# Kernel optimization log

Measured on AMD Instinct MI355X. Metric: run time of the kernel, lower is better.

## Reference

```python
import jax, jax.numpy as jnp
import numpy as np
import math

T, B, D, H, FF = 2048, 2, 1024, 16, 4096
HD = D // H
STD = 0.02


def _gelu(x):
    # SongNet gelu: tanh approximation
    return 0.5 * x * (1.0 + jnp.tanh(math.sqrt(2.0 / math.pi) * (x + 0.044715 * x ** 3)))


def _layer_norm(x, g, b, eps=1e-5):
    mu = jnp.mean(x, axis=-1, keepdims=True)
    var = jnp.mean((x - mu) ** 2, axis=-1, keepdims=True)
    return (x - mu) * jax.lax.rsqrt(var + eps) * g + b


def setup_inputs() -> dict:
    key = jax.random.key(0)
    ks = jax.random.split(key, 6)
    return {
        "x": jax.random.normal(ks[0], (T, B, D), jnp.float32),
        "attn_mask": jnp.triu(jnp.ones((T, T), bool), k=1),  # True = masked (causal)
        "in_proj_w": jax.random.normal(ks[1], (3 * D, D), jnp.float32) * STD,
        "in_proj_b": jnp.zeros((3 * D,), jnp.float32),
        "out_w": jax.random.normal(ks[2], (D, D), jnp.float32) * STD,
        "out_b": jnp.zeros((D,), jnp.float32),
        "fc1_w": jax.random.normal(ks[3], (FF, D), jnp.float32) * STD,
        "fc1_b": jnp.zeros((FF,), jnp.float32),
        "fc2_w": jax.random.normal(ks[4], (D, FF), jnp.float32) * STD,
        "fc2_b": jnp.zeros((D,), jnp.float32),
        "ln1_g": jnp.ones((D,), jnp.float32),
        "ln1_b": jnp.zeros((D,), jnp.float32),
        "ln2_g": jnp.ones((D,), jnp.float32),
        "ln2_b": jnp.zeros((D,), jnp.float32),
    }


def reference(x, attn_mask, in_proj_w, in_proj_b, out_w, out_b,
              fc1_w, fc1_b, fc2_w, fc2_b, ln1_g, ln1_b, ln2_g, ln2_b):
    t, b, d = x.shape
    scaling = HD ** -0.5
    # fused in-proj (qkv_same path): [T,B,3D]
    qkv = x @ in_proj_w.T + in_proj_b
    q, k, v = jnp.split(qkv, 3, axis=-1)
    q = q * scaling

    def to_heads(z):  # [T,B,D] -> [B*H, T, HD]
        return z.reshape(t, b * H, HD).transpose(1, 0, 2)

    q, k, v = to_heads(q), to_heads(k), to_heads(v)
    # [B*H, T, T] attention scores (full matrix, as in original bmm)
    scores = jnp.einsum('nth,nsh->nts', q, k)
    scores = jnp.where(attn_mask[None, :, :], -jnp.inf, scores)
    w = jax.nn.softmax(scores, axis=-1)
    attn = jnp.einsum('nts,nsh->nth', w, v)          # [B*H, T, HD]
    attn = attn.transpose(1, 0, 2).reshape(t, b, d)  # [T,B,D]
    attn = attn @ out_w.T + out_b

    h = _layer_norm(x + attn, ln1_g, ln1_b)
    ff = _gelu(h @ fc1_w.T + fc1_b) @ fc2_w.T + fc2_b
    out = _layer_norm(h + ff, ln2_g, ln2_b)
    return out
```

## Files before the change

### kernel.cpp

```cpp
#include <hip/hip_runtime.h>
#include <hip/hip_bf16.h>
#include <math.h>


typedef __bf16 bf16x8_t __attribute__((ext_vector_type(8)));
typedef __bf16 bf16x4_t __attribute__((ext_vector_type(4)));
typedef __bf16 bf16x2_t __attribute__((ext_vector_type(2)));
typedef float  f32x4_t  __attribute__((ext_vector_type(4)));

#define T_  2048
#define B_  2
#define D_  1024
#define H_  16
#define HD_ 64
#define FF_ 4096
#define M_  (T_ * B_)

#define LOG2E 1.4426950408889634f
#define SCL   (0.125f * LOG2E)

__device__ __forceinline__ float gelu_f(float v) {
    const float y = 0.79788456080286535588f * (v + 0.044715f * v * v * v);
    const float t = __builtin_amdgcn_exp2f(-2.8853900817779268f * y);
    return v * __builtin_amdgcn_rcpf(1.0f + t);
}

__device__ __forceinline__ void gld_lds16(const void* g, void* l) {
    __builtin_amdgcn_global_load_lds((const __attribute__((address_space(1))) void*)g,
                                     (__attribute__((address_space(3))) void*)l, 16, 0, 0);
}

template<int MODE, int OWNM, int VT>
__global__ __launch_bounds__(256, 4)
void gemm_bt(const __bf16* __restrict__ A, const __bf16* __restrict__ W,
             const float* __restrict__ bias, float* __restrict__ Cf0,
             float* __restrict__ Cf1, __bf16* __restrict__ Cb,
             __bf16* __restrict__ vt, int M, int N, int K)
{
    __shared__ __align__(16) __bf16 As[128 * 64];
    __shared__ __align__(16) __bf16 Bs[128 * 64];
    const int tid  = threadIdx.x;
    const int lane = tid & 63;
    const int wave = tid >> 6;
    const int quad = lane >> 4;
    const int l15  = lane & 15;

    const int gx = gridDim.x, gy = gridDim.y;
    int flat = ((int)blockIdx.z * gy + (int)blockIdx.y) * gx + (int)blockIdx.x;
    int bx, by, z;
    if (OWNM) {
        const int P = gy >> 3;
        const int x = flat & 7; int s = flat >> 3;
        by = x * P + (s % P); s /= P;
        bx = s % gx; z = s / gx;
    } else {
        const int P = gx >> 3;
        const int x = flat & 7; int s = flat >> 3;
        bx = x * P + (s % P); s /= P;
        by = s % gy; z = s / gy;
    }
    const int m0 = by * 128;
    const int n0 = bx * 128;
    const int wm = (wave >> 1) * 64;
    const int wn = (wave & 1) * 64;
    const int Kloc = K / (int)gridDim.z;
    const int kbeg = z * Kloc;

    const int srow8 = lane >> 3;
    const int scol  = ((lane & 7) ^ srow8) * 8;
    const __bf16* gA = A + (size_t)(m0 + wave * 32 + srow8) * K + scol;
    const __bf16* gB = W + (size_t)(n0 + wave * 32 + srow8) * K + scol;
    const size_t row8K = (size_t)8 * K;
    __bf16* ldsA = As + wave * 2048;
    __bf16* ldsB = Bs + wave * 2048;

    const int fsw = l15 & 7;

    f32x4_t acc[4][4] = {};

    for (int kb = kbeg; kb < kbeg + Kloc; kb += 64) {
        #pragma unroll
        for (int j = 0; j < 4; ++j) {
            gld_lds16(gA + kb + j * row8K, ldsA + j * 512);
            gld_lds16(gB + kb + j * row8K, ldsB + j * 512);
        }
        __syncthreads();
        #pragma unroll
        for (int half = 0; half < 2; ++half) {
            const int co = ((quad + half * 4) ^ fsw) * 8;
            bf16x8_t af[4], bfr[4];
            #pragma unroll
            for (int i = 0; i < 4; ++i) af[i]  = *(const bf16x8_t*)&As[(wm + i * 16 + l15) * 64 + co];
            #pragma unroll
            for (int i = 0; i < 4; ++i) bfr[i] = *(const bf16x8_t*)&Bs[(wn + i * 16 + l15) * 64 + co];
            #pragma unroll
            for (int mi = 0; mi < 4; ++mi)
                #pragma unroll
                for (int ni = 0; ni < 4; ++ni)
                    acc[mi][ni] = __builtin_amdgcn_mfma_f32_16x16x32_bf16(af[mi], bfr[ni], acc[mi][ni], 0, 0, 0);
        }
        __syncthreads();
    }

    float* __restrict__ Cf = (z == 0) ? Cf0 : Cf1;
    #pragma unroll
    for (int mi = 0; mi < 4; ++mi) {
        const int row = m0 + wm + mi * 16 + quad * 4;
        #pragma unroll
        for (int ni = 0; ni < 4; ++ni) {
            const int col = n0 + wn + ni * 16 + l15;
            const float bv = (z == 0) ? bias[col] : 0.f;
            float v[4];
            #pragma unroll
            for (int r = 0; r < 4; ++r) {
                v[r] = acc[mi][ni][r] + bv;
                if (MODE == 2) v[r] = gelu_f(v[r]);
            }
            if (MODE == 0) {
                #pragma unroll
                for (int r = 0; r < 4; ++r) Cf[(size_t)(row + r) * N + col] = v[r];
            } else {
                #pragma unroll
                for (int r = 0; r < 4; ++r) Cb[(size_t)(row + r) * N + col] = (__bf16)v[r];
            }
            if (VT && n0 >= 2 * D_) {
                const int colv = col - 2 * D_;
                const int h2 = colv >> 6, hd = colv & 63;
                const int t0 = row >> 1;
                bf16x2_t p0 = {(__bf16)v[0], (__bf16)v[2]};
                bf16x2_t p1 = {(__bf16)v[1], (__bf16)v[3]};
                *(bf16x2_t*)(vt + ((size_t)(h2 * 64 + hd)) * T_ + t0) = p0;
                *(bf16x2_t*)(vt + ((size_t)((H_ + h2) * 64 + hd)) * T_ + t0) = p1;
            }
        }
    }
}

struct QState {
    bf16x8_t aq0, aq1;
    f32x4_t  o[4];
    float    lsum;
};

__device__ __forceinline__ void attn_tile_step(
    QState& st, const __bf16* __restrict__ Ks, const __bf16* __restrict__ Vs,
    __bf16* __restrict__ Psw, bool diag, int wave, int quad, int l15, int ksw)
{
    f32x4_t scT[4] = {};
    #pragma unroll
    for (int ni = 0; ni < 4; ++ni) {
        const int rb = (ni * 16 + l15) * 64;
        bf16x8_t kf0 = *(const bf16x8_t*)&Ks[rb + ((quad ^ ksw) & 7) * 8];
        bf16x8_t kf1 = *(const bf16x8_t*)&Ks[rb + (((quad + 4) ^ ksw) & 7) * 8];
        scT[ni] = __builtin_amdgcn_mfma_f32_16x16x32_bf16(kf0, st.aq0, scT[ni], 0, 0, 0);
        scT[ni] = __builtin_amdgcn_mfma_f32_16x16x32_bf16(kf1, st.aq1, scT[ni], 0, 0, 0);
    }
    float rsum = 0.f;
    #pragma unroll
    for (int ni = 0; ni < 4; ++ni) {
        bf16x4_t pk;
        #pragma unroll
        for (int r = 0; r < 4; ++r) {
            float pv = __builtin_amdgcn_exp2f(scT[ni][r] * SCL);
            if (diag) {
                const int sl = ni * 16 + quad * 4 + r;
                pv = (sl <= wave * 16 + l15) ? pv : 0.f;
            }
            rsum += pv;
            pk[r] = (__bf16)pv;
        }
        *(bf16x4_t*)&Psw[l15 * 64 + ((ni * 4 + quad + l15) & 15) * 4] = pk;
    }
    rsum += __shfl_xor(rsum, 16, 64);
    rsum += __shfl_xor(rsum, 32, 64);
    st.lsum += rsum;

    const int rowb = l15 * 64;
    bf16x4_t a0 = *(const bf16x4_t*)&Psw[rowb + ((quad * 2     + l15) & 15) * 4];
    bf16x4_t a1 = *(const bf16x4_t*)&Psw[rowb + ((quad * 2 + 1 + l15) & 15) * 4];
    bf16x4_t a2 = *(const bf16x4_t*)&Psw[rowb + ((quad * 2 + 8 + l15) & 15) * 4];
    bf16x4_t a3 = *(const bf16x4_t*)&Psw[rowb + ((quad * 2 + 9 + l15) & 15) * 4];
    bf16x8_t ap0 = __builtin_shufflevector(a0, a1, 0, 1, 2, 3, 4, 5, 6, 7);
    bf16x8_t ap1 = __builtin_shufflevector(a2, a3, 0, 1, 2, 3, 4, 5, 6, 7);

    #pragma unroll
    for (int ni = 0; ni < 4; ++ni) {
        const int rbv = (ni * 16 + l15) * 64;
        bf16x8_t bv0 = *(const bf16x8_t*)&Vs[rbv + ((quad ^ ksw) & 7) * 8];
        bf16x8_t bv1 = *(const bf16x8_t*)&Vs[rbv + (((quad + 4) ^ ksw) & 7) * 8];
        st.o[ni] = __builtin_amdgcn_mfma_f32_16x16x32_bf16(ap0, bv0, st.o[ni], 0, 0, 0);
        st.o[ni] = __builtin_amdgcn_mfma_f32_16x16x32_bf16(ap1, bv1, st.o[ni], 0, 0, 0);
    }
}

__global__ __launch_bounds__(256)
void attn_kernel(const __bf16* __restrict__ qkv, const __bf16* __restrict__ vt,
                 __bf16* __restrict__ attnout)
{
    const int bh = blockIdx.y;
    const int b  = bh >> 4;
    const int h  = bh & 15;
    const int tid  = threadIdx.x;
    const int lane = tid & 63;
    const int wave = tid >> 6;
    const int quad = lane >> 4;
    const int l15  = lane & 15;

    __shared__ __align__(16) __bf16 Ks[64 * 64];
    __shared__ __align__(16) __bf16 Vs[64 * 64];
    __shared__ __align__(16) __bf16 Ps[4][16 * 64];

    const int kr = lane >> 3;
    const int kc = (lane & 7) ^ kr;
    const size_t krow = (size_t)B_ * 3 * D_;
    const __bf16* gK0 = qkv + ((size_t)(wave * 16 + kr) * B_ + b) * (3 * D_) + D_ + h * HD_ + kc * 8;
    const __bf16* gV0 = vt + ((size_t)bh * 64 + wave * 16 + kr) * T_ + kc * 8;
    __bf16* ldsK0 = &Ks[wave * 16 * 64];
    __bf16* ldsK1 = &Ks[wave * 16 * 64 + 8 * 64];
    __bf16* ldsV0 = &Vs[wave * 16 * 64];
    __bf16* ldsV1 = &Vs[wave * 16 * 64 + 8 * 64];
    const int ksw = l15 & 7;
    __bf16* Psw = &Ps[wave][0];

    const int qtA = 31 - (int)blockIdx.x;
    const int qtB = (int)blockIdx.x;

    QState stA = {}, stB = {};
    {
        const int tqA = qtA * 64 + wave * 16 + l15;
        const __bf16* qbA = qkv + ((size_t)tqA * B_ + b) * (3 * D_) + h * HD_;
        stA.aq0 = *(const bf16x8_t*)(qbA + quad * 8);
        stA.aq1 = *(const bf16x8_t*)(qbA + 32 + quad * 8);
        const int tqB = qtB * 64 + wave * 16 + l15;
        const __bf16* qbB = qkv + ((size_t)tqB * B_ + b) * (3 * D_) + h * HD_;
        stB.aq0 = *(const bf16x8_t*)(qbB + quad * 8);
        stB.aq1 = *(const bf16x8_t*)(qbB + 32 + quad * 8);
    }

    for (int kt = 0; kt <= qtA; ++kt) {
        const int s0 = kt * 64;
        __syncthreads();
        gld_lds16(gK0 + (size_t)s0 * krow,       ldsK0);
        gld_lds16(gK0 + (size_t)(s0 + 8) * krow, ldsK1);
        gld_lds16(gV0 + s0,                      ldsV0);
        gld_lds16(gV0 + (size_t)8 * T_ + s0,     ldsV1);
        __syncthreads();

        attn_tile_step(stA, Ks, Vs, Psw, kt == qtA, wave, quad, l15, ksw);
        if (kt <= qtB)
            attn_tile_step(stB, Ks, Vs, Psw, kt == qtB, wave, quad, l15, ksw);
    }

    #pragma unroll
    for (int t = 0; t < 2; ++t) {
        const QState& st = t ? stB : stA;
        const int q0 = (t ? qtB : qtA) * 64;
        float linv[4];
        #pragma unroll
        for (int r = 0; r < 4; ++r)
            linv[r] = __builtin_amdgcn_rcpf(__shfl(st.lsum, quad * 4 + r, 64));
        #pragma unroll
        for (int ni = 0; ni < 4; ++ni) {
            #pragma unroll
            for (int r = 0; r < 4; ++r) {
                const int tr = q0 + wave * 16 + quad * 4 + r;
                attnout[((size_t)tr * B_ + b) * D_ + h * HD_ + ni * 16 + l15] =
                    (__bf16)(st.o[ni][r] * linv[r]);
            }
        }
    }
}

template<int AF32, int WF, int WB>
__global__ __launch_bounds__(256)
void ln3_kernel(const void* __restrict__ Ap, const float* __restrict__ R0,
                const float* __restrict__ R1,
                const float* __restrict__ g, const float* __restrict__ bb,
                float* __restrict__ outf, __bf16* __restrict__ outb)
{
    const int row = blockIdx.x;
    const int tid = threadIdx.x;
    float a0, a1, a2, a3;
    if (AF32) {
        const float4 va = ((const float4*)((const float*)Ap + (size_t)row * D_))[tid];
        a0 = va.x; a1 = va.y; a2 = va.z; a3 = va.w;
    } else {
        const bf16x4_t va = ((const bf16x4_t*)((const __bf16*)Ap + (size_t)row * D_))[tid];
        a0 = (float)va[0]; a1 = (float)va[1]; a2 = (float)va[2]; a3 = (float)va[3];
    }
    const float4 v0 = ((const float4*)(R0 + (size_t)row * D_))[tid];
    const float4 v1 = ((const float4*)(R1 + (size_t)row * D_))[tid];
    const float z0 = a0 + v0.x + v1.x, z1 = a1 + v0.y + v1.y;
    const float z2 = a2 + v0.z + v1.z, z3 = a3 + v0.w + v1.w;
    float s  = z0 + z1 + z2 + z3;
    float ss = z0 * z0 + z1 * z1 + z2 * z2 + z3 * z3;
    #pragma unroll
    for (int off = 1; off < 64; off <<= 1) {
        s  += __shfl_xor(s, off, 64);
        ss += __shfl_xor(ss, off, 64);
    }
    __shared__ float rs[4], rss[4];
    const int wv = tid >> 6, lane = tid & 63;
    if (lane == 0) { rs[wv] = s; rss[wv] = ss; }
    __syncthreads();
    s  = rs[0] + rs[1] + rs[2] + rs[3];
    ss = rss[0] + rss[1] + rss[2] + rss[3];
    const float mu   = s * (1.f / D_);
    const float var  = ss * (1.f / D_) - mu * mu;
    const float rstd = rsqrtf(var + 1e-5f);
    const float4 vg = ((const float4*)g)[tid];
    const float4 vb = ((const float4*)bb)[tid];
    const float o0 = (z0 - mu) * rstd * vg.x + vb.x;
    const float o1 = (z1 - mu) * rstd * vg.y + vb.y;
    const float o2 = (z2 - mu) * rstd * vg.z + vb.z;
    const float o3 = (z3 - mu) * rstd * vg.w + vb.w;
    if (WF) ((float4*)(outf + (size_t)row * D_))[tid] = make_float4(o0, o1, o2, o3);
    if (WB) {
        bf16x4_t ob;
        ob[0] = (__bf16)o0; ob[1] = (__bf16)o1; ob[2] = (__bf16)o2; ob[3] = (__bf16)o3;
        ((bf16x4_t*)(outb + (size_t)row * D_))[tid] = ob;
    }
}

__global__ __launch_bounds__(256)
void cvt3_kernel(const float* __restrict__ s0, __bf16* __restrict__ d0, int n0,
                 const float* __restrict__ s1, __bf16* __restrict__ d1, int n1,
                 const float* __restrict__ s2, __bf16* __restrict__ d2, int n2)
{
    int i = blockIdx.x * 256 + threadIdx.x;
    const float* s; __bf16* d;
    if (i < n0) { s = s0; d = d0; }
    else if ((i -= n0) < n1) { s = s1; d = d1; }
    else if ((i -= n1) < n2) { s = s2; d = d2; }
    else return;
    const float4 v = ((const float4*)s)[i];
    bf16x4_t ob;
    ob[0] = (__bf16)v.x; ob[1] = (__bf16)v.y; ob[2] = (__bf16)v.z; ob[3] = (__bf16)v.w;
    ((bf16x4_t*)d)[i] = ob;
}

extern "C" void kernel_launch(void* const* d_in, const int* in_sizes, int n_in,
                              void* d_out, int out_size, void* d_ws, size_t ws_size,
                              hipStream_t stream)
{
    (void)in_sizes; (void)n_in; (void)out_size; (void)ws_size;
    const float* x         = (const float*)d_in[0];
    const float* in_proj_w = (const float*)d_in[2];
    const float* in_proj_b = (const float*)d_in[3];
    const float* out_w     = (const float*)d_in[4];
    const float* out_b     = (const float*)d_in[5];
    const float* fc1_w     = (const float*)d_in[6];
    const float* fc1_b     = (const float*)d_in[7];
    const float* fc2_w     = (const float*)d_in[8];
    const float* fc2_b     = (const float*)d_in[9];
    const float* ln1_g     = (const float*)d_in[10];
    const float* ln1_b     = (const float*)d_in[11];
    const float* ln2_g     = (const float*)d_in[12];
    const float* ln2_b     = (const float*)d_in[13];

    char* p = (char*)d_ws;
    __bf16* regA = (__bf16*)p; p += (size_t)M_ * D_ * 2;
    __bf16* hb   = (__bf16*)p; p += (size_t)M_ * D_ * 2;
    __bf16* wreg = (__bf16*)p; p += (size_t)FF_ * D_ * 2;
    __bf16* qkvb = (__bf16*)p;
    __bf16* g1b  = qkvb;       p += (size_t)M_ * FF_ * 2;
    float*  yf   = (float*)p;  p += (size_t)M_ * D_ * 4;
    float*  hf   = (float*)p;  p += (size_t)M_ * D_ * 4;
    __bf16* vt    = (__bf16*)yf;
    __bf16* outwb = wreg + (size_t)3 * D_ * D_;
    __bf16* fc2wb = (__bf16*)hf;
    float*  ff1   = (float*)d_out;

    const dim3 blk(256);

    {
        const int nx = M_ * D_ / 4, ni = 3 * D_ * D_ / 4, no = D_ * D_ / 4;
        cvt3_kernel<<<dim3((nx + ni + no) / 256), blk, 0, stream>>>(
            x, regA, nx, in_proj_w, wreg, ni, out_w, outwb, no);
    }

    gemm_bt<1, 1, 1><<<dim3(3 * D_ / 128, M_ / 128, 1), blk, 0, stream>>>(
        regA, wreg, in_proj_b, nullptr, nullptr, qkvb, vt, M_, 3 * D_, D_);

    attn_kernel<<<dim3(T_ / 128, B_ * H_), blk, 0, stream>>>(qkvb, vt, regA);

    gemm_bt<0, 1, 0><<<dim3(D_ / 128, M_ / 128, 2), blk, 0, stream>>>(
        regA, outwb, out_b, yf, hf, nullptr, nullptr, M_, D_, D_);

    ln3_kernel<1, 0, 1><<<dim3(M_), blk, 0, stream>>>(x, yf, hf, ln1_g, ln1_b, nullptr, hb);

    cvt3_kernel<<<dim3((2 * FF_ * D_ / 4) / 256), blk, 0, stream>>>(
        fc1_w, wreg, FF_ * D_ / 4, fc2_w, fc2wb, D_ * FF_ / 4, nullptr, nullptr, 0);

    gemm_bt<2, 0, 0><<<dim3(FF_ / 128, M_ / 128, 1), blk, 0, stream>>>(
        hb, wreg, fc1_b, nullptr, nullptr, g1b, nullptr, M_, FF_, D_);

    gemm_bt<0, 1, 0><<<dim3(D_ / 128, M_ / 128, 2), blk, 0, stream>>>(
        g1b, fc2wb, fc2_b, yf, ff1, nullptr, nullptr, M_, D_, FF_);

    ln3_kernel<0, 1, 0><<<dim3(M_), blk, 0, stream>>>(hb, yf, ff1, ln2_g, ln2_b, (float*)d_out, nullptr);
}
```

Baseline: 329.1 us.

## Double-buffer K/V tiles and interleave both query tiles per attention step

The attention kernel now keeps two LDS buffers for K and V. While the current tile is being computed, it prefetches the next tile, which removes the second barrier and the exposed global-to-LDS load latency in each iteration. The two per-block query tiles (A and B) are also processed together in one fused step with separate P scratch buffers. Their independent MFMA and exp chains can then interleave for more instruction-level parallelism. The cost is twice the LDS for K, V and P and more live registers, which may reduce occupancy.

After: 335.6 us. About the same (+2.0%).

```diff
diff --git a/kernel.cpp b/kernel.cpp
--- a/kernel.cpp
+++ b/kernel.cpp
@@ -142,54 +142,97 @@
     float    lsum;
 };
 
-__device__ __forceinline__ void attn_tile_step(
-    QState& st, const __bf16* __restrict__ Ks, const __bf16* __restrict__ Vs,
-    __bf16* __restrict__ Psw, bool diag, int wave, int quad, int l15, int ksw)
-{
-    f32x4_t scT[4] = {};
+__device__ __forceinline__ void attn_dual_step(
+    QState& stA, QState& stB, bool doB, bool diagA, bool diagB,
+    const __bf16* __restrict__ Ks, const __bf16* __restrict__ Vs,
+    __bf16* __restrict__ PsA, __bf16* __restrict__ PsB,
+    int wave, int quad, int l15, int ksw)
+{
+    f32x4_t scA[4] = {}, scB[4] = {};
     #pragma unroll
     for (int ni = 0; ni < 4; ++ni) {
         const int rb = (ni * 16 + l15) * 64;
         bf16x8_t kf0 = *(const bf16x8_t*)&Ks[rb + ((quad ^ ksw) & 7) * 8];
         bf16x8_t kf1 = *(const bf16x8_t*)&Ks[rb + (((quad + 4) ^ ksw) & 7) * 8];
-        scT[ni] = __builtin_amdgcn_mfma_f32_16x16x32_bf16(kf0, st.aq0, scT[ni], 0, 0, 0);
-        scT[ni] = __builtin_amdgcn_mfma_f32_16x16x32_bf16(kf1, st.aq1, scT[ni], 0, 0, 0);
-    }
-    float rsum = 0.f;
+        scA[ni] = __builtin_amdgcn_mfma_f32_16x16x32_bf16(kf0, stA.aq0, scA[ni], 0, 0, 0);
+        scA[ni] = __builtin_amdgcn_mfma_f32_16x16x32_bf16(kf1, stA.aq1, scA[ni], 0, 0, 0);
+        if (doB) {
+            scB[ni] = __builtin_amdgcn_mfma_f32_16x16x32_bf16(kf0, stB.aq0, scB[ni], 0, 0, 0);
+            scB[ni] = __builtin_amdgcn_mfma_f32_16x16x32_bf16(kf1, stB.aq1, scB[ni], 0, 0, 0);
+        }
+    }
+    float rsumA = 0.f, rsumB = 0.f;
     #pragma unroll
     for (int ni = 0; ni < 4; ++ni) {
-        bf16x4_t pk;
+        const int slot = ((ni * 4 + quad + l15) & 15) * 4;
+        bf16x4_t pkA;
         #pragma unroll
         for (int r = 0; r < 4; ++r) {
-            float pv = __builtin_amdgcn_exp2f(scT[ni][r] * SCL);
-            if (diag) {
+            float pv = __builtin_amdgcn_exp2f(scA[ni][r] * SCL);
+            if (diagA) {
                 const int sl = ni * 16 + quad * 4 + r;
                 pv = (sl <= wave * 16 + l15) ? pv : 0.f;
             }
-            rsum += pv;
-            pk[r] = (__bf16)pv;
-        }
-        *(bf16x4_t*)&Psw[l15 * 64 + ((ni * 4 + quad + l15) & 15) * 4] = pk;
-    }
-    rsum += __shfl_xor(rsum, 16, 64);
-    rsum += __shfl_xor(rsum, 32, 64);
-    st.lsum += rsum;
+            rsumA += pv;
+            pkA[r] = (__bf16)pv;
+        }
+        *(bf16x4_t*)&PsA[l15 * 64 + slot] = pkA;
+        if (doB) {
+            bf16x4_t pkB;
+            #pragma unroll
+            for (int r = 0; r < 4; ++r) {
+                float pv = __builtin_amdgcn_exp2f(scB[ni][r] * SCL);
+                if (diagB) {
+                    const int sl = ni * 16 + quad * 4 + r;
+                    pv = (sl <= wave * 16 + l15) ? pv : 0.f;
+                }
+                rsumB += pv;
+                pkB[r] = (__bf16)pv;
+            }
+            *(bf16x4_t*)&PsB[l15 * 64 + slot] = pkB;
+        }
+    }
+    rsumA += __shfl_xor(rsumA, 16, 64);
+    rsumA += __shfl_xor(rsumA, 32, 64);
+    stA.lsum += rsumA;
+    if (doB) {
+        rsumB += __shfl_xor(rsumB, 16, 64);
+        rsumB += __shfl_xor(rsumB, 32, 64);
+        stB.lsum += rsumB;
+    }
 
     const int rowb = l15 * 64;
-    bf16x4_t a0 = *(const bf16x4_t*)&Psw[rowb + ((quad * 2     + l15) & 15) * 4];
-    bf16x4_t a1 = *(const bf16x4_t*)&Psw[rowb + ((quad * 2 + 1 + l15) & 15) * 4];
-    bf16x4_t a2 = *(const bf16x4_t*)&Psw[rowb + ((quad * 2 + 8 + l15) & 15) * 4];
-    bf16x4_t a3 = *(const bf16x4_t*)&Psw[rowb + ((quad * 2 + 9 + l15) & 15) * 4];
-    bf16x8_t ap0 = __builtin_shufflevector(a0, a1, 0, 1, 2, 3, 4, 5, 6, 7);
-    bf16x8_t ap1 = __builtin_shufflevector(a2, a3, 0, 1, 2, 3, 4, 5, 6, 7);
+    const int c0 = ((quad * 2     + l15) & 15) * 4;
+    const int c1 = ((quad * 2 + 1 + l15) & 15) * 4;
+    const int c2 = ((quad * 2 + 8 + l15) & 15) * 4;
+    const int c3 = ((quad * 2 + 9 + l15) & 15) * 4;
+    bf16x4_t a0 = *(const bf16x4_t*)&PsA[rowb + c0];
+    bf16x4_t a1 = *(const bf16x4_t*)&PsA[rowb + c1];
+    bf16x4_t a2 = *(const bf16x4_t*)&PsA[rowb + c2];
+    bf16x4_t a3 = *(const bf16x4_t*)&PsA[rowb + c3];
+    bf16x8_t apA0 = __builtin_shufflevector(a0, a1, 0, 1, 2, 3, 4, 5, 6, 7);
+    bf16x8_t apA1 = __builtin_shufflevector(a2, a3, 0, 1, 2, 3, 4, 5, 6, 7);
+    bf16x8_t apB0, apB1;
+    if (doB) {
+        bf16x4_t b0 = *(const bf16x4_t*)&PsB[rowb + c0];
+        bf16x4_t b1 = *(const bf16x4_t*)&PsB[rowb + c1];
+        bf16x4_t b2 = *(const bf16x4_t*)&PsB[rowb + c2];
+        bf16x4_t b3 = *(const bf16x4_t*)&PsB[rowb + c3];
+        apB0 = __builtin_shufflevector(b0, b1, 0, 1, 2, 3, 4, 5, 6, 7);
+        apB1 = __builtin_shufflevector(b2, b3, 0, 1, 2, 3, 4, 5, 6, 7);
+    }
 
     #pragma unroll
     for (int ni = 0; ni < 4; ++ni) {
         const int rbv = (ni * 16 + l15) * 64;
         bf16x8_t bv0 = *(const bf16x8_t*)&Vs[rbv + ((quad ^ ksw) & 7) * 8];
         bf16x8_t bv1 = *(const bf16x8_t*)&Vs[rbv + (((quad + 4) ^ ksw) & 7) * 8];
-        st.o[ni] = __builtin_amdgcn_mfma_f32_16x16x32_bf16(ap0, bv0, st.o[ni], 0, 0, 0);
-        st.o[ni] = __builtin_amdgcn_mfma_f32_16x16x32_bf16(ap1, bv1, st.o[ni], 0, 0, 0);
+        stA.o[ni] = __builtin_amdgcn_mfma_f32_16x16x32_bf16(apA0, bv0, stA.o[ni], 0, 0, 0);
+        stA.o[ni] = __builtin_amdgcn_mfma_f32_16x16x32_bf16(apA1, bv1, stA.o[ni], 0, 0, 0);
+        if (doB) {
+            stB.o[ni] = __builtin_amdgcn_mfma_f32_16x16x32_bf16(apB0, bv0, stB.o[ni], 0, 0, 0);
+            stB.o[ni] = __builtin_amdgcn_mfma_f32_16x16x32_bf16(apB1, bv1, stB.o[ni], 0, 0, 0);
+        }
     }
 }
 
@@ -206,21 +249,18 @@
     const int quad = lane >> 4;
     const int l15  = lane & 15;
 
-    __shared__ __align__(16) __bf16 Ks[64 * 64];
-    __shared__ __align__(16) __bf16 Vs[64 * 64];
-    __shared__ __align__(16) __bf16 Ps[4][16 * 64];
+    __shared__ __align__(16) __bf16 Ks[2][64 * 64];
+    __shared__ __align__(16) __bf16 Vs[2][64 * 64];
+    __shared__ __align__(16) __bf16 Ps[2][4][16 * 64];
 
     const int kr = lane >> 3;
     const int kc = (lane & 7) ^ kr;
     const size_t krow = (size_t)B_ * 3 * D_;
     const __bf16* gK0 = qkv + ((size_t)(wave * 16 + kr) * B_ + b) * (3 * D_) + D_ + h * HD_ + kc * 8;
     const __bf16* gV0 = vt + ((size_t)bh * 64 + wave * 16 + kr) * T_ + kc * 8;
-    __bf16* ldsK0 = &Ks[wave * 16 * 64];
-    __bf16* ldsK1 = &Ks[wave * 16 * 64 + 8 * 64];
-    __bf16* ldsV0 = &Vs[wave * 16 * 64];
-    __bf16* ldsV1 = &Vs[wave * 16 * 64 + 8 * 64];
     const int ksw = l15 & 7;
-    __bf16* Psw = &Ps[wave][0];
+    __bf16* PsA = &Ps[0][wave][0];
+    __bf16* PsB = &Ps[1][wave][0];
 
     const int qtA = 31 - (int)blockIdx.x;
     const int qtB = (int)blockIdx.x;
@@ -237,18 +277,30 @@
         stB.aq1 = *(const bf16x8_t*)(qbB + 32 + quad * 8);
     }
 
+    {
+        __bf16* k0 = &Ks[0][wave * 16 * 64];
+        __bf16* v0 = &Vs[0][wave * 16 * 64];
+        gld_lds16(gK0,                  k0);
+        gld_lds16(gK0 + (size_t)8 * krow, k0 + 8 * 64);
+        gld_lds16(gV0,                  v0);
+        gld_lds16(gV0 + (size_t)8 * T_, v0 + 8 * 64);
+    }
+
     for (int kt = 0; kt <= qtA; ++kt) {
-        const int s0 = kt * 64;
         __syncthreads();
-        gld_lds16(gK0 + (size_t)s0 * krow,       ldsK0);
-        gld_lds16(gK0 + (size_t)(s0 + 8) * krow, ldsK1);
-        gld_lds16(gV0 + s0,                      ldsV0);
-        gld_lds16(gV0 + (size_t)8 * T_ + s0,     ldsV1);
-        __syncthreads();
-
-        attn_tile_step(stA, Ks, Vs, Psw, kt == qtA, wave, quad, l15, ksw);
-        if (kt <= qtB)
-            attn_tile_step(stB, Ks, Vs, Psw, kt == qtB, wave, quad, l15, ksw);
+        if (kt < qtA) {
+            const int s1 = (kt + 1) * 64;
+            const int bi = (kt + 1) & 1;
+            __bf16* k1 = &Ks[bi][wave * 16 * 64];
+            __bf16* v1 = &Vs[bi][wave * 16 * 64];
+            gld_lds16(gK0 + (size_t)s1 * krow,       k1);
+            gld_lds16(gK0 + (size_t)(s1 + 8) * krow, k1 + 8 * 64);
+            gld_lds16(gV0 + s1,                      v1);
+            gld_lds16(gV0 + (size_t)8 * T_ + s1,     v1 + 8 * 64);
+        }
+        attn_dual_step(stA, stB, kt <= qtB, kt == qtA, kt == qtB,
+                       &Ks[kt & 1][0], &Vs[kt & 1][0], PsA, PsB,
+                       wave, quad, l15, ksw);
     }
 
     #pragma unroll
```
